# Optimization experiments

Hardware: AMD Instinct MI355X
Metric: run time of the kernel (lower is better)

The kernel has to match this reference:

```python
import jax, jax.numpy as jnp
import numpy as np

NEG = -10000000.0

def setup_inputs() -> dict:
    key0 = jax.random.key(0)
    ks = jax.random.split(key0, 5)
    B, XL, KL, D = 16, 1024, 512, 1024  # D = 2*rnn_dim
    return {
        "x": jax.random.normal(ks[0], (B, XL, D), dtype=jnp.float32),
        "x_mask": jnp.ones((B, XL), dtype=jnp.float32),
        "key": jax.random.normal(ks[1], (B, KL, D), dtype=jnp.float32),
        "key_mask": jnp.ones((B, KL), dtype=jnp.float32),
        "w_input": jax.random.normal(ks[2], (D,), dtype=jnp.float32) / np.sqrt(D),
        "w_key": jax.random.normal(ks[3], (D,), dtype=jnp.float32) / np.sqrt(D),
        "dot_w": jax.random.normal(ks[4], (D,), dtype=jnp.float32) / np.sqrt(D),
    }

def reference(x, x_mask, key, key_mask, w_input, w_key, dot_w):
    # Trilinear attention score S[b,i,j] = w_in.x_i + w_key.k_j + (x_i*dot_w).k_j
    x_logits = jnp.einsum('bxd,d->bx', x, w_input)      # [B, XL]
    key_logits = jnp.einsum('bkd,d->bk', key, w_key)    # [B, KL]
    S = (x_logits[:, :, None] + key_logits[:, None, :]
         + jnp.einsum('bxd,bkd->bxk', x * dot_w, key))  # [B, XL, KL]

    # x -> key attention with joint mask
    joint_mask = 1.0 - x_mask[:, :, None] * key_mask[:, None, :]
    masked_S = S + joint_mask * NEG
    attn = jax.nn.softmax(masked_S, axis=-1)
    x2key = jnp.einsum('bxk,bkd->bxd', attn, key)       # [B, XL, D]

    # key -> x attention: mask over key dim, max-reduce, masked softmax over x
    km = key_mask[:, None, :]
    S2 = S * km + (1.0 - km) * NEG                      # add_masked_value
    max_s = jnp.max(S2, axis=-1)                        # [B, XL]
    p = jax.nn.softmax(max_s * x_mask, axis=-1) * x_mask  # claf masked_softmax
    p = p / (jnp.sum(p, axis=-1, keepdims=True) + 1e-13)
    key2x = jnp.einsum('bx,bxd->bd', p, x)[:, None, :]  # [B, 1, D], broadcasts

    key2x_full = jnp.broadcast_to(key2x, x.shape)
    return jnp.concatenate([x, x2key, x * x2key, x * key2x_full], axis=-1)
```

## Files before the change

### kernel.cpp

```cpp
#include <hip/hip_runtime.h>
#include <hip/hip_fp16.h>

#define B_ 16
#define XL_ 1024
#define KL_ 512
#define D_ 1024
#define NEGC (-10000000.0f)

typedef _Float16 f16x8 __attribute__((ext_vector_type(8)));
typedef float f32x4 __attribute__((ext_vector_type(4)));
typedef unsigned short u16x8 __attribute__((ext_vector_type(8)));
typedef unsigned short u16x4 __attribute__((ext_vector_type(4)));

__device__ __forceinline__ unsigned short f2h(float f) {
  __half h = __float2half(f);
  return __half_as_ushort(h);
}

__global__ __launch_bounds__(256) void k_build(const float* __restrict__ key,
    const float* __restrict__ w_key, unsigned short* __restrict__ KQ2,
    unsigned short* __restrict__ KV2, float* __restrict__ klog) {
  __shared__ unsigned short tile[64][72];
  int bid = blockIdx.x;
  int b = bid >> 4;
  int ks = (bid >> 1) & 7;
  int dh = bid & 1;
  int tid = threadIdx.x;
  int kr = tid >> 2;
  int cq = tid & 3;
  const float* krow = key + ((size_t)(b * KL_ + ks * 64 + kr)) * D_;
  float klacc = 0.f;
  int dl = tid & 63, g = tid >> 6;

  for (int dt = dh * 8; dt < dh * 8 + 8; ++dt) {
#pragma unroll
    for (int j = 0; j < 4; ++j) {
      int c = dt * 64 + cq * 16 + j * 4;
      float4 v = *(const float4*)(krow + c);
      float4 w = *(const float4*)(w_key + c);
      klacc += v.x * w.x + v.y * w.y + v.z * w.z + v.w * w.w;
      u16x4 hv;
      hv[0] = f2h(v.x); hv[1] = f2h(v.y); hv[2] = f2h(v.z); hv[3] = f2h(v.w);
      *(u16x4*)(&tile[kr][cq * 16 + j * 4]) = hv;
    }
    __syncthreads();
#pragma unroll
    for (int dkc_l = 0; dkc_l < 2; ++dkc_l) {
      u16x8 hv = *(const u16x8*)(&tile[kr][dkc_l * 32 + cq * 8]);
      size_t dst = (((size_t)(b * 8 + ks) * 32 + (dt * 2 + dkc_l)) << 11)
                   + (size_t)(((kr >> 4) & 3) * 512 + (cq * 16 + (kr & 15)) * 8);
      *(u16x8*)(KQ2 + dst) = hv;
    }
    {
      int dglob = dt * 64 + dl;
      int wv_ = dglob >> 7, np = (dglob >> 4) & 7, l15v = dglob & 15;
#pragma unroll
      for (int kkc_l = 0; kkc_l < 2; ++kkc_l) {
        u16x8 hv;
#pragma unroll
        for (int h = 0; h < 8; ++h) hv[h] = tile[kkc_l * 32 + g * 8 + h][dl];
        size_t dst = (((size_t)(b * 8 + wv_) * 16 + (ks * 2 + kkc_l)) << 12)
                     + (size_t)(np * 512 + (g * 16 + l15v) * 8);
        *(u16x8*)(KV2 + dst) = hv;
      }
    }
    __syncthreads();
  }
  klacc += __shfl_xor(klacc, 1);
  klacc += __shfl_xor(klacc, 2);
  if (cq == 0) atomicAdd(&klog[b * KL_ + ks * 64 + kr], klacc);
}

__global__ __launch_bounds__(512, 4) void k_attn(
    const float* __restrict__ x, const float* __restrict__ x_mask,
    const float* __restrict__ key_mask, const float* __restrict__ dot_w,
    const float* __restrict__ w_input,
    const unsigned short* __restrict__ KQ2, const unsigned short* __restrict__ KV2,
    const float* __restrict__ klog,
    float* __restrict__ maxs, float* __restrict__ out) {
  __shared__ unsigned short Qall[32 * 1024];
  __shared__ float xlg[32];
  unsigned short* Pt = Qall;
  float* redA = (float*)(Qall + 16384);
  float* redB = redA + 256;
  float* redC = redB + 256;

  const int tid = threadIdx.x;
  const int wv = tid >> 6;
  const int lane = tid & 63;
  const int l15 = lane & 15, l4 = lane >> 4;
  const int r7 = l15 & 7;

  int bid = blockIdx.x;
  int b = (bid & 7) * 2 + (bid >> 8);
  int x0 = ((bid >> 3) & 31) * 32;

  const float* xB = x + ((size_t)b * XL_ + x0) * D_;

  {
    int row = tid >> 4;
    int cg = tid & 15;
    const float* sp = xB + (size_t)row * D_;
    float* outx = out + ((size_t)b * XL_ + x0 + row) * (size_t)(4 * D_);
    char* qrow = (char*)Qall + row * 2048;
    int rsw = row & 7;
    float xl = 0.f;
#pragma unroll
    for (int j = 0; j < 16; ++j) {
      int c4 = cg + j * 16;
      f32x4 v = *(const f32x4*)(sp + c4 * 4);
      f32x4 w = *(const f32x4*)(dot_w + c4 * 4);
      f32x4 wi = *(const f32x4*)(w_input + c4 * 4);
      xl += v[0] * wi[0] + v[1] * wi[1] + v[2] * wi[2] + v[3] * wi[3];
      __builtin_nontemporal_store(v, (f32x4*)(outx + c4 * 4));
      u16x4 hv;
      hv[0] = f2h(v[0] * w[0]); hv[1] = f2h(v[1] * w[1]);
      hv[2] = f2h(v[2] * w[2]); hv[3] = f2h(v[3] * w[3]);
      *(u16x4*)(qrow + (((c4 >> 1) ^ rsw) << 4) + ((c4 & 1) << 3)) = hv;
    }
    xl += __shfl_xor(xl, 1);
    xl += __shfl_xor(xl, 2);
    xl += __shfl_xor(xl, 4);
    xl += __shfl_xor(xl, 8);
    if (cg == 0) xlg[row] = xl;
  }
  __syncthreads();

  f32x4 acc[2][4];
#pragma unroll
  for (int m = 0; m < 2; ++m)
#pragma unroll
    for (int n = 0; n < 4; ++n) { f32x4 z = {0.f, 0.f, 0.f, 0.f}; acc[m][n] = z; }

  const unsigned short* KQ2w = KQ2 + (((size_t)(b * 8 + wv) * 32) << 11) + lane * 8;
  const char* qa0 = (char*)Qall + l15 * 2048;
  const char* qa1 = (char*)Qall + (16 + l15) * 2048;

#pragma unroll 4
  for (int dk = 0; dk < D_; dk += 32) {
    const unsigned short* cp = KQ2w + ((dk >> 5) << 11);
    f16x8 b0 = *(const f16x8*)(cp);
    f16x8 b1 = *(const f16x8*)(cp + 512);
    f16x8 b2 = *(const f16x8*)(cp + 1024);
    f16x8 b3 = *(const f16x8*)(cp + 1536);
    int c = (((dk >> 3) + l4) ^ r7) << 4;
    f16x8 a0 = *(const f16x8*)(qa0 + c);
    f16x8 a1 = *(const f16x8*)(qa1 + c);
    __builtin_amdgcn_s_setprio(1);
    acc[0][0] = __builtin_amdgcn_mfma_f32_16x16x32_f16(b0, a0, acc[0][0], 0, 0, 0);
    acc[1][0] = __builtin_amdgcn_mfma_f32_16x16x32_f16(b0, a1, acc[1][0], 0, 0, 0);
    acc[0][1] = __builtin_amdgcn_mfma_f32_16x16x32_f16(b1, a0, acc[0][1], 0, 0, 0);
    acc[1][1] = __builtin_amdgcn_mfma_f32_16x16x32_f16(b1, a1, acc[1][1], 0, 0, 0);
    acc[0][2] = __builtin_amdgcn_mfma_f32_16x16x32_f16(b2, a0, acc[0][2], 0, 0, 0);
    acc[1][2] = __builtin_amdgcn_mfma_f32_16x16x32_f16(b2, a1, acc[1][2], 0, 0, 0);
    acc[0][3] = __builtin_amdgcn_mfma_f32_16x16x32_f16(b3, a0, acc[0][3], 0, 0, 0);
    acc[1][3] = __builtin_amdgcn_mfma_f32_16x16x32_f16(b3, a1, acc[1][3], 0, 0, 0);
    __builtin_amdgcn_s_setprio(0);
  }
  __syncthreads();

  float xlv[2], xmv[2];
#pragma unroll
  for (int m = 0; m < 2; ++m) {
    int row = m * 16 + l15;
    xlv[m] = xlg[row];
    xmv[m] = x_mask[(size_t)b * XL_ + x0 + row];
  }
  f32x4 klv[4], kmv[4];
#pragma unroll
  for (int n = 0; n < 4; ++n) {
    int kb = wv * 64 + n * 16 + l4 * 4;
    klv[n] = *(const f32x4*)(klog + (size_t)b * KL_ + kb);
    kmv[n] = *(const f32x4*)(key_mask + (size_t)b * KL_ + kb);
  }
  float mxsm[2] = {-3.0e38f, -3.0e38f}, mxs2[2] = {-3.0e38f, -3.0e38f};
#pragma unroll
  for (int m = 0; m < 2; ++m)
#pragma unroll
    for (int n = 0; n < 4; ++n)
#pragma unroll
      for (int q = 0; q < 4; ++q) {
        float s = acc[m][n][q] + xlv[m] + klv[n][q];
        float sm = s + (1.f - xmv[m] * kmv[n][q]) * NEGC;
        float s2 = s * kmv[n][q] + (1.f - kmv[n][q]) * NEGC;
        mxsm[m] = fmaxf(mxsm[m], sm);
        mxs2[m] = fmaxf(mxs2[m], s2);
      }
#pragma unroll
  for (int m = 0; m < 2; ++m) {
    mxsm[m] = fmaxf(mxsm[m], __shfl_xor(mxsm[m], 16));
    mxsm[m] = fmaxf(mxsm[m], __shfl_xor(mxsm[m], 32));
    mxs2[m] = fmaxf(mxs2[m], __shfl_xor(mxs2[m], 16));
    mxs2[m] = fmaxf(mxs2[m], __shfl_xor(mxs2[m], 32));
  }
  if (l4 == 0) {
#pragma unroll
    for (int m = 0; m < 2; ++m) {
      redA[wv * 32 + m * 16 + l15] = mxsm[m];
      redB[wv * 32 + m * 16 + l15] = mxs2[m];
    }
  }
  __syncthreads();
  float gmx[2];
#pragma unroll
  for (int m = 0; m < 2; ++m) {
    int row = m * 16 + l15;
    float v = redA[row];
#pragma unroll
    for (int w = 1; w < 8; ++w) v = fmaxf(v, redA[w * 32 + row]);
    gmx[m] = v;
  }
  if (tid < 32) {
    float v = redB[tid];
#pragma unroll
    for (int w = 1; w < 8; ++w) v = fmaxf(v, redB[w * 32 + tid]);
    maxs[(size_t)b * XL_ + x0 + tid] = v;
  }
  float rs[2] = {0.f, 0.f};
#pragma unroll
  for (int m = 0; m < 2; ++m) {
    int row = m * 16 + l15;
    char* prow = (char*)Pt + row * 1024;
    int rsw = row & 7;
#pragma unroll
    for (int n = 0; n < 4; ++n) {
      int k = wv * 64 + n * 16 + l4 * 4;
      u16x4 pk;
#pragma unroll
      for (int q = 0; q < 4; ++q) {
        float s = acc[m][n][q] + xlv[m] + klv[n][q];
        float sm = s + (1.f - xmv[m] * kmv[n][q]) * NEGC;
        float e = __expf(sm - gmx[m]);
        rs[m] += e;
        pk[q] = f2h(e);
      }
      *(u16x4*)(prow + ((((k >> 3) ^ rsw) << 4) + ((k & 4) << 1))) = pk;
    }
  }
#pragma unroll
  for (int m = 0; m < 2; ++m) {
    rs[m] += __shfl_xor(rs[m], 16);
    rs[m] += __shfl_xor(rs[m], 32);
  }
  if (l4 == 0) {
#pragma unroll
    for (int m = 0; m < 2; ++m) redC[wv * 32 + m * 16 + l15] = rs[m];
  }
  __syncthreads();

  float dn[2];
#pragma unroll
  for (int m = 0; m < 2; ++m) {
    int row = m * 16 + l15;
    float sum = redC[row];
#pragma unroll
    for (int w = 1; w < 8; ++w) sum += redC[w * 32 + row];
    dn[m] = 1.f / sum;
  }
  size_t obase0 = ((size_t)b * XL_ + x0) * (size_t)(4 * D_);
  const char* pa0 = (char*)Pt + l15 * 1024;
  const char* pa1 = (char*)Pt + (16 + l15) * 1024;
  const unsigned short* KV2w = KV2 + (((size_t)(b * 8 + wv) * 16) << 12) + lane * 8;
#pragma unroll
  for (int sc = 0; sc < 2; ++sc) {
    int c0 = wv * 128 + sc * 64;
    f32x4 acc2[2][4];
#pragma unroll
    for (int m = 0; m < 2; ++m)
#pragma unroll
      for (int n = 0; n < 4; ++n) { f32x4 z = {0.f, 0.f, 0.f, 0.f}; acc2[m][n] = z; }
    const unsigned short* KV2s = KV2w + sc * 4 * 512;
#pragma unroll 4
    for (int kk = 0; kk < KL_; kk += 32) {
      const unsigned short* cp = KV2s + ((kk >> 5) << 12);
      f16x8 b0 = *(const f16x8*)(cp);
      f16x8 b1 = *(const f16x8*)(cp + 512);
      f16x8 b2 = *(const f16x8*)(cp + 1024);
      f16x8 b3 = *(const f16x8*)(cp + 1536);
      int c = ((((kk >> 3) + l4) ^ r7) << 4);
      f16x8 a0 = *(const f16x8*)(pa0 + c);
      f16x8 a1 = *(const f16x8*)(pa1 + c);
      __builtin_amdgcn_s_setprio(1);
      acc2[0][0] = __builtin_amdgcn_mfma_f32_16x16x32_f16(b0, a0, acc2[0][0], 0, 0, 0);
      acc2[1][0] = __builtin_amdgcn_mfma_f32_16x16x32_f16(b0, a1, acc2[1][0], 0, 0, 0);
      acc2[0][1] = __builtin_amdgcn_mfma_f32_16x16x32_f16(b1, a0, acc2[0][1], 0, 0, 0);
      acc2[1][1] = __builtin_amdgcn_mfma_f32_16x16x32_f16(b1, a1, acc2[1][1], 0, 0, 0);
      acc2[0][2] = __builtin_amdgcn_mfma_f32_16x16x32_f16(b2, a0, acc2[0][2], 0, 0, 0);
      acc2[1][2] = __builtin_amdgcn_mfma_f32_16x16x32_f16(b2, a1, acc2[1][2], 0, 0, 0);
      acc2[0][3] = __builtin_amdgcn_mfma_f32_16x16x32_f16(b3, a0, acc2[0][3], 0, 0, 0);
      acc2[1][3] = __builtin_amdgcn_mfma_f32_16x16x32_f16(b3, a1, acc2[1][3], 0, 0, 0);
      __builtin_amdgcn_s_setprio(0);
    }
#pragma unroll
    for (int m = 0; m < 2; ++m) {
      int row = m * 16 + l15;
      size_t ob = obase0 + (size_t)row * (4 * D_);
      const float* xr = xB + (size_t)row * D_;
#pragma unroll
      for (int n = 0; n < 4; ++n) {
        int col = c0 + n * 16 + l4 * 4;
        f32x4 v = acc2[m][n];
        v[0] *= dn[m]; v[1] *= dn[m]; v[2] *= dn[m]; v[3] *= dn[m];
        f32x4 xv = *(const f32x4*)(xr + col);
        __builtin_nontemporal_store(v, (f32x4*)(out + ob + D_ + col));
        f32x4 pv;
        pv[0] = v[0] * xv[0]; pv[1] = v[1] * xv[1];
        pv[2] = v[2] * xv[2]; pv[3] = v[3] * xv[3];
        __builtin_nontemporal_store(pv, (f32x4*)(out + ob + 2 * D_ + col));
      }
    }
  }
}

__global__ __launch_bounds__(256) void k_key2x_part(const float* __restrict__ x,
    const float* __restrict__ maxs, const float* __restrict__ x_mask,
    float* __restrict__ partial) {
  int b = blockIdx.x >> 4;
  int xc = blockIdx.x & 15;
  int tid = threadIdx.x;
  int wvi = tid >> 6, lane = tid & 63;
  __shared__ float r1[4], r2[4], r3[4];
  __shared__ float ps_all[XL_];
  const float* ms = maxs + (size_t)b * XL_;
  const float* xm = x_mask + (size_t)b * XL_;
  float tv[4], xmv[4];
  float vmax = -3.0e38f;
#pragma unroll
  for (int i = 0; i < 4; ++i) {
    int xi = i * 256 + tid;
    xmv[i] = xm[xi];
    tv[i] = ms[xi] * xmv[i];
    vmax = fmaxf(vmax, tv[i]);
  }
#pragma unroll
  for (int sh = 32; sh >= 1; sh >>= 1) vmax = fmaxf(vmax, __shfl_xor(vmax, sh));
  if (lane == 0) r1[wvi] = vmax;
  __syncthreads();
  float gmax = fmaxf(fmaxf(r1[0], r1[1]), fmaxf(r1[2], r1[3]));
  float e[4]; float es = 0.f;
#pragma unroll
  for (int i = 0; i < 4; ++i) { e[i] = __expf(tv[i] - gmax); es += e[i]; }
#pragma unroll
  for (int sh = 32; sh >= 1; sh >>= 1) es += __shfl_xor(es, sh);
  if (lane == 0) r2[wvi] = es;
  __syncthreads();
  float gsum = r2[0] + r2[1] + r2[2] + r2[3];
  float pv4[4]; float psum = 0.f;
#pragma unroll
  for (int i = 0; i < 4; ++i) { pv4[i] = e[i] / gsum * xmv[i]; psum += pv4[i]; }
#pragma unroll
  for (int sh = 32; sh >= 1; sh >>= 1) psum += __shfl_xor(psum, sh);
  if (lane == 0) r3[wvi] = psum;
  __syncthreads();
  float gps = r3[0] + r3[1] + r3[2] + r3[3];
  float inv = 1.f / (gps + 1e-13f);
#pragma unroll
  for (int i = 0; i < 4; ++i) ps_all[i * 256 + tid] = pv4[i] * inv;
  __syncthreads();
  const float* xb = x + ((size_t)b * XL_ + xc * 64) * D_;
  float acc0 = 0.f, acc1 = 0.f, acc2 = 0.f, acc3 = 0.f;
  int d = tid;
  const float* psl = ps_all + xc * 64;
  for (int xi = 0; xi < 64; ++xi) {
    float pv = psl[xi];
    const float* rp = xb + (size_t)xi * D_;
    acc0 += pv * __builtin_nontemporal_load(rp + d);
    acc1 += pv * __builtin_nontemporal_load(rp + d + 256);
    acc2 += pv * __builtin_nontemporal_load(rp + d + 512);
    acc3 += pv * __builtin_nontemporal_load(rp + d + 768);
  }
  float* pp = partial + (size_t)blockIdx.x * D_;
  pp[d] = acc0; pp[d + 256] = acc1; pp[d + 512] = acc2; pp[d + 768] = acc3;
}

__global__ __launch_bounds__(256) void k_key2x_red(const float* __restrict__ partial,
    float* __restrict__ k2x) {
  int idx = blockIdx.x * 256 + threadIdx.x;
  int b = idx >> 10;
  float s = 0.f;
#pragma unroll
  for (int xc = 0; xc < 16; ++xc)
    s += partial[((size_t)b * 16 + xc) * D_ + (idx & 1023)];
  k2x[idx] = s;
}

__global__ __launch_bounds__(256) void k_outfinal(const float* __restrict__ x,
    const float* __restrict__ k2x, float* __restrict__ out) {
  size_t t = (size_t)blockIdx.x * 256 + threadIdx.x;
  size_t base = t * 4;
  int b = (int)(base >> 20);
  int rem = (int)(base & ((1u << 20) - 1));
  int xr = rem >> 10;
  int d = rem & 1023;
  f32x4 xv = __builtin_nontemporal_load((const f32x4*)(x + base));
  f32x4 kv = *(const f32x4*)(k2x + (size_t)b * D_ + d);
  float* orow = out + ((size_t)b * XL_ + xr) * (size_t)(4 * D_);
  f32x4 pr;
  pr[0] = xv[0] * kv[0]; pr[1] = xv[1] * kv[1];
  pr[2] = xv[2] * kv[2]; pr[3] = xv[3] * kv[3];
  __builtin_nontemporal_store(pr, (f32x4*)(orow + 3 * D_ + d));
}

extern "C" void kernel_launch(void* const* d_in, const int* in_sizes, int n_in,
                              void* d_out, int out_size, void* d_ws, size_t ws_size,
                              hipStream_t stream) {
  (void)in_sizes; (void)n_in; (void)out_size; (void)ws_size;
  const float* x        = (const float*)d_in[0];
  const float* x_mask   = (const float*)d_in[1];
  const float* key      = (const float*)d_in[2];
  const float* key_mask = (const float*)d_in[3];
  const float* w_input  = (const float*)d_in[4];
  const float* w_key    = (const float*)d_in[5];
  const float* dot_w    = (const float*)d_in[6];
  float* out = (float*)d_out;
  char* ws = (char*)d_ws;

  unsigned short* KQ2 = (unsigned short*)ws;
  unsigned short* KV2 = (unsigned short*)(ws + (16u << 20));
  float* xlog = (float*)(ws + (32u << 20));
  float* klog = xlog + B_ * XL_;
  float* maxs = klog + B_ * KL_;
  float* pbuf = maxs + B_ * XL_;
  float* k2x  = pbuf + B_ * XL_;
  float* partial = (float*)ws;

  hipMemsetAsync(klog, 0, B_ * KL_ * sizeof(float), stream);
  k_build<<<dim3(B_ * 16), dim3(256), 0, stream>>>(key, w_key, KQ2, KV2, klog);
  k_attn<<<dim3(512), dim3(512), 0, stream>>>(x, x_mask, key_mask, dot_w, w_input,
                                              KQ2, KV2, klog, maxs, out);
  k_key2x_part<<<dim3(B_ * 16), dim3(256), 0, stream>>>(x, maxs, x_mask, partial);
  k_key2x_red<<<dim3(B_ * D_ / 256), dim3(256), 0, stream>>>(partial, k2x);
  k_outfinal<<<dim3(B_ * XL_ * D_ / 1024), dim3(256), 0, stream>>>(x, k2x, out);
}
```

Before: 172.8 us.

## Double attention block rows to 64 and move x copy into epilogue

Each k_attn block now handles 64 query rows instead of 32, so every K fragment loaded from global memory feeds four MFMA row tiles instead of two. This halves the grid to 256 blocks and doubles shared memory and accumulator registers, with launch bounds lowered to 2 blocks per CU. The copy of x into the first output slice moves from the prologue into the x2key epilogue, reusing the x values already loaded there. The nontemporal stores become ordinary stores. The larger tile risks register pressure and lower occupancy, and 256 blocks may leave some CUs idle.

Result: slower. 184.8 us (+6.9%).

```diff
diff --git a/kernel.cpp b/kernel.cpp
--- a/kernel.cpp
+++ b/kernel.cpp
@@ -71,19 +71,19 @@
   if (cq == 0) atomicAdd(&klog[b * KL_ + ks * 64 + kr], klacc);
 }
 
-__global__ __launch_bounds__(512, 4) void k_attn(
+__global__ __launch_bounds__(512, 2) void k_attn(
     const float* __restrict__ x, const float* __restrict__ x_mask,
     const float* __restrict__ key_mask, const float* __restrict__ dot_w,
     const float* __restrict__ w_input,
     const unsigned short* __restrict__ KQ2, const unsigned short* __restrict__ KV2,
     const float* __restrict__ klog,
     float* __restrict__ maxs, float* __restrict__ out) {
-  __shared__ unsigned short Qall[32 * 1024];
-  __shared__ float xlg[32];
+  __shared__ unsigned short Qall[64 * 1024];
+  __shared__ float xlg[64];
   unsigned short* Pt = Qall;
-  float* redA = (float*)(Qall + 16384);
-  float* redB = redA + 256;
-  float* redC = redB + 256;
+  float* redA = (float*)((char*)Qall + 65536);
+  float* redB = redA + 512;
+  float* redC = redB + 512;
 
   const int tid = threadIdx.x;
   const int wv = tid >> 6;
@@ -92,27 +92,25 @@
   const int r7 = l15 & 7;
 
   int bid = blockIdx.x;
-  int b = (bid & 7) * 2 + (bid >> 8);
-  int x0 = ((bid >> 3) & 31) * 32;
+  int b = (bid & 7) * 2 + (bid >> 7);
+  int x0 = ((bid >> 3) & 15) * 64;
 
   const float* xB = x + ((size_t)b * XL_ + x0) * D_;
 
   {
-    int row = tid >> 4;
-    int cg = tid & 15;
+    int row = tid >> 3;
+    int cg = tid & 7;
     const float* sp = xB + (size_t)row * D_;
-    float* outx = out + ((size_t)b * XL_ + x0 + row) * (size_t)(4 * D_);
     char* qrow = (char*)Qall + row * 2048;
     int rsw = row & 7;
     float xl = 0.f;
 #pragma unroll
-    for (int j = 0; j < 16; ++j) {
-      int c4 = cg + j * 16;
+    for (int j = 0; j < 32; ++j) {
+      int c4 = cg + j * 8;
       f32x4 v = *(const f32x4*)(sp + c4 * 4);
       f32x4 w = *(const f32x4*)(dot_w + c4 * 4);
       f32x4 wi = *(const f32x4*)(w_input + c4 * 4);
       xl += v[0] * wi[0] + v[1] * wi[1] + v[2] * wi[2] + v[3] * wi[3];
-      __builtin_nontemporal_store(v, (f32x4*)(outx + c4 * 4));
       u16x4 hv;
       hv[0] = f2h(v[0] * w[0]); hv[1] = f2h(v[1] * w[1]);
       hv[2] = f2h(v[2] * w[2]); hv[3] = f2h(v[3] * w[3]);
@@ -121,22 +119,23 @@
     xl += __shfl_xor(xl, 1);
     xl += __shfl_xor(xl, 2);
     xl += __shfl_xor(xl, 4);
-    xl += __shfl_xor(xl, 8);
     if (cg == 0) xlg[row] = xl;
   }
   __syncthreads();
 
-  f32x4 acc[2][4];
-#pragma unroll
-  for (int m = 0; m < 2; ++m)
+  f32x4 acc[4][4];
+#pragma unroll
+  for (int m = 0; m < 4; ++m)
 #pragma unroll
     for (int n = 0; n < 4; ++n) { f32x4 z = {0.f, 0.f, 0.f, 0.f}; acc[m][n] = z; }
 
   const unsigned short* KQ2w = KQ2 + (((size_t)(b * 8 + wv) * 32) << 11) + lane * 8;
   const char* qa0 = (char*)Qall + l15 * 2048;
   const char* qa1 = (char*)Qall + (16 + l15) * 2048;
-
-#pragma unroll 4
+  const char* qa2 = (char*)Qall + (32 + l15) * 2048;
+  const char* qa3 = (char*)Qall + (48 + l15) * 2048;
+
+#pragma unroll 2
   for (int dk = 0; dk < D_; dk += 32) {
     const unsigned short* cp = KQ2w + ((dk >> 5) << 11);
     f16x8 b0 = *(const f16x8*)(cp);
@@ -146,22 +145,32 @@
     int c = (((dk >> 3) + l4) ^ r7) << 4;
     f16x8 a0 = *(const f16x8*)(qa0 + c);
     f16x8 a1 = *(const f16x8*)(qa1 + c);
+    f16x8 a2 = *(const f16x8*)(qa2 + c);
+    f16x8 a3 = *(const f16x8*)(qa3 + c);
     __builtin_amdgcn_s_setprio(1);
     acc[0][0] = __builtin_amdgcn_mfma_f32_16x16x32_f16(b0, a0, acc[0][0], 0, 0, 0);
     acc[1][0] = __builtin_amdgcn_mfma_f32_16x16x32_f16(b0, a1, acc[1][0], 0, 0, 0);
+    acc[2][0] = __builtin_amdgcn_mfma_f32_16x16x32_f16(b0, a2, acc[2][0], 0, 0, 0);
+    acc[3][0] = __builtin_amdgcn_mfma_f32_16x16x32_f16(b0, a3, acc[3][0], 0, 0, 0);
     acc[0][1] = __builtin_amdgcn_mfma_f32_16x16x32_f16(b1, a0, acc[0][1], 0, 0, 0);
     acc[1][1] = __builtin_amdgcn_mfma_f32_16x16x32_f16(b1, a1, acc[1][1], 0, 0, 0);
+    acc[2][1] = __builtin_amdgcn_mfma_f32_16x16x32_f16(b1, a2, acc[2][1], 0, 0, 0);
+    acc[3][1] = __builtin_amdgcn_mfma_f32_16x16x32_f16(b1, a3, acc[3][1], 0, 0, 0);
     acc[0][2] = __builtin_amdgcn_mfma_f32_16x16x32_f16(b2, a0, acc[0][2], 0, 0, 0);
     acc[1][2] = __builtin_amdgcn_mfma_f32_16x16x32_f16(b2, a1, acc[1][2], 0, 0, 0);
+    acc[2][2] = __builtin_amdgcn_mfma_f32_16x16x32_f16(b2, a2, acc[2][2], 0, 0, 0);
+    acc[3][2] = __builtin_amdgcn_mfma_f32_16x16x32_f16(b2, a3, acc[3][2], 0, 0, 0);
     acc[0][3] = __builtin_amdgcn_mfma_f32_16x16x32_f16(b3, a0, acc[0][3], 0, 0, 0);
     acc[1][3] = __builtin_amdgcn_mfma_f32_16x16x32_f16(b3, a1, acc[1][3], 0, 0, 0);
+    acc[2][3] = __builtin_amdgcn_mfma_f32_16x16x32_f16(b3, a2, acc[2][3], 0, 0, 0);
+    acc[3][3] = __builtin_amdgcn_mfma_f32_16x16x32_f16(b3, a3, acc[3][3], 0, 0, 0);
     __builtin_amdgcn_s_setprio(0);
   }
   __syncthreads();
 
-  float xlv[2], xmv[2];
-#pragma unroll
-  for (int m = 0; m < 2; ++m) {
+  float xlv[4], xmv[4];
+#pragma unroll
+  for (int m = 0; m < 4; ++m) {
     int row = m * 16 + l15;
     xlv[m] = xlg[row];
     xmv[m] = x_mask[(size_t)b * XL_ + x0 + row];
@@ -173,9 +182,11 @@
     klv[n] = *(const f32x4*)(klog + (size_t)b * KL_ + kb);
     kmv[n] = *(const f32x4*)(key_mask + (size_t)b * KL_ + kb);
   }
-  float mxsm[2] = {-3.0e38f, -3.0e38f}, mxs2[2] = {-3.0e38f, -3.0e38f};
-#pragma unroll
-  for (int m = 0; m < 2; ++m)
+  float mxsm[4], mxs2[4];
+#pragma unroll
+  for (int m = 0; m < 4; ++m) { mxsm[m] = -3.0e38f; mxs2[m] = -3.0e38f; }
+#pragma unroll
+  for (int m = 0; m < 4; ++m)
 #pragma unroll
     for (int n = 0; n < 4; ++n)
 #pragma unroll
@@ -187,7 +198,7 @@
         mxs2[m] = fmaxf(mxs2[m], s2);
       }
 #pragma unroll
-  for (int m = 0; m < 2; ++m) {
+  for (int m = 0; m < 4; ++m) {
     mxsm[m] = fmaxf(mxsm[m], __shfl_xor(mxsm[m], 16));
     mxsm[m] = fmaxf(mxsm[m], __shfl_xor(mxsm[m], 32));
     mxs2[m] = fmaxf(mxs2[m], __shfl_xor(mxs2[m], 16));
@@ -195,30 +206,30 @@
   }
   if (l4 == 0) {
 #pragma unroll
-    for (int m = 0; m < 2; ++m) {
-      redA[wv * 32 + m * 16 + l15] = mxsm[m];
-      redB[wv * 32 + m * 16 + l15] = mxs2[m];
-    }
-  }
-  __syncthreads();
-  float gmx[2];
-#pragma unroll
-  for (int m = 0; m < 2; ++m) {
+    for (int m = 0; m < 4; ++m) {
+      redA[wv * 64 + m * 16 + l15] = mxsm[m];
+      redB[wv * 64 + m * 16 + l15] = mxs2[m];
+    }
+  }
+  __syncthreads();
+  float gmx[4];
+#pragma unroll
+  for (int m = 0; m < 4; ++m) {
     int row = m * 16 + l15;
     float v = redA[row];
 #pragma unroll
-    for (int w = 1; w < 8; ++w) v = fmaxf(v, redA[w * 32 + row]);
+    for (int w = 1; w < 8; ++w) v = fmaxf(v, redA[w * 64 + row]);
     gmx[m] = v;
   }
-  if (tid < 32) {
+  if (tid < 64) {
     float v = redB[tid];
 #pragma unroll
-    for (int w = 1; w < 8; ++w) v = fmaxf(v, redB[w * 32 + tid]);
+    for (int w = 1; w < 8; ++w) v = fmaxf(v, redB[w * 64 + tid]);
     maxs[(size_t)b * XL_ + x0 + tid] = v;
   }
-  float rs[2] = {0.f, 0.f};
-#pragma unroll
-  for (int m = 0; m < 2; ++m) {
+  float rs[4] = {0.f, 0.f, 0.f, 0.f};
+#pragma unroll
+  for (int m = 0; m < 4; ++m) {
     int row = m * 16 + l15;
     char* prow = (char*)Pt + row * 1024;
     int rsw = row & 7;
@@ -238,39 +249,41 @@
     }
   }
 #pragma unroll
-  for (int m = 0; m < 2; ++m) {
+  for (int m = 0; m < 4; ++m) {
     rs[m] += __shfl_xor(rs[m], 16);
     rs[m] += __shfl_xor(rs[m], 32);
   }
   if (l4 == 0) {
 #pragma unroll
-    for (int m = 0; m < 2; ++m) redC[wv * 32 + m * 16 + l15] = rs[m];
-  }
-  __syncthreads();
-
-  float dn[2];
-#pragma unroll
-  for (int m = 0; m < 2; ++m) {
+    for (int m = 0; m < 4; ++m) redC[wv * 64 + m * 16 + l15] = rs[m];
+  }
+  __syncthreads();
+
+  float dn[4];
+#pragma unroll
+  for (int m = 0; m < 4; ++m) {
     int row = m * 16 + l15;
     float sum = redC[row];
 #pragma unroll
-    for (int w = 1; w < 8; ++w) sum += redC[w * 32 + row];
+    for (int w = 1; w < 8; ++w) sum += redC[w * 64 + row];
     dn[m] = 1.f / sum;
   }
   size_t obase0 = ((size_t)b * XL_ + x0) * (size_t)(4 * D_);
   const char* pa0 = (char*)Pt + l15 * 1024;
   const char* pa1 = (char*)Pt + (16 + l15) * 1024;
+  const char* pa2 = (char*)Pt + (32 + l15) * 1024;
+  const char* pa3 = (char*)Pt + (48 + l15) * 1024;
   const unsigned short* KV2w = KV2 + (((size_t)(b * 8 + wv) * 16) << 12) + lane * 8;
 #pragma unroll
   for (int sc = 0; sc < 2; ++sc) {
     int c0 = wv * 128 + sc * 64;
-    f32x4 acc2[2][4];
-#pragma unroll
-    for (int m = 0; m < 2; ++m)
+    f32x4 acc2[4][4];
+#pragma unroll
+    for (int m = 0; m < 4; ++m)
 #pragma unroll
       for (int n = 0; n < 4; ++n) { f32x4 z = {0.f, 0.f, 0.f, 0.f}; acc2[m][n] = z; }
     const unsigned short* KV2s = KV2w + sc * 4 * 512;
-#pragma unroll 4
+#pragma unroll 2
     for (int kk = 0; kk < KL_; kk += 32) {
       const unsigned short* cp = KV2s + ((kk >> 5) << 12);
       f16x8 b0 = *(const f16x8*)(cp);
@@ -280,19 +293,29 @@
       int c = ((((kk >> 3) + l4) ^ r7) << 4);
       f16x8 a0 = *(const f16x8*)(pa0 + c);
       f16x8 a1 = *(const f16x8*)(pa1 + c);
+      f16x8 a2 = *(const f16x8*)(pa2 + c);
+      f16x8 a3 = *(const f16x8*)(pa3 + c);
       __builtin_amdgcn_s_setprio(1);
       acc2[0][0] = __builtin_amdgcn_mfma_f32_16x16x32_f16(b0, a0, acc2[0][0], 0, 0, 0);
       acc2[1][0] = __builtin_amdgcn_mfma_f32_16x16x32_f16(b0, a1, acc2[1][0], 0, 0, 0);
+      acc2[2][0] = __builtin_amdgcn_mfma_f32_16x16x32_f16(b0, a2, acc2[2][0], 0, 0, 0);
+      acc2[3][0] = __builtin_amdgcn_mfma_f32_16x16x32_f16(b0, a3, acc2[3][0], 0, 0, 0);
       acc2[0][1] = __builtin_amdgcn_mfma_f32_16x16x32_f16(b1, a0, acc2[0][1], 0, 0, 0);
       acc2[1][1] = __builtin_amdgcn_mfma_f32_16x16x32_f16(b1, a1, acc2[1][1], 0, 0, 0);
+      acc2[2][1] = __builtin_amdgcn_mfma_f32_16x16x32_f16(b1, a2, acc2[2][1], 0, 0, 0);
+      acc2[3][1] = __builtin_amdgcn_mfma_f32_16x16x32_f16(b1, a3, acc2[3][1], 0, 0, 0);
       acc2[0][2] = __builtin_amdgcn_mfma_f32_16x16x32_f16(b2, a0, acc2[0][2], 0, 0, 0);
       acc2[1][2] = __builtin_amdgcn_mfma_f32_16x16x32_f16(b2, a1, acc2[1][2], 0, 0, 0);
+      acc2[2][2] = __builtin_amdgcn_mfma_f32_16x16x32_f16(b2, a2, acc2[2][2], 0, 0, 0);
+      acc2[3][2] = __builtin_amdgcn_mfma_f32_16x16x32_f16(b2, a3, acc2[3][2], 0, 0, 0);
       acc2[0][3] = __builtin_amdgcn_mfma_f32_16x16x32_f16(b3, a0, acc2[0][3], 0, 0, 0);
       acc2[1][3] = __builtin_amdgcn_mfma_f32_16x16x32_f16(b3, a1, acc2[1][3], 0, 0, 0);
+      acc2[2][3] = __builtin_amdgcn_mfma_f32_16x16x32_f16(b3, a2, acc2[2][3], 0, 0, 0);
+      acc2[3][3] = __builtin_amdgcn_mfma_f32_16x16x32_f16(b3, a3, acc2[3][3], 0, 0, 0);
       __builtin_amdgcn_s_setprio(0);
     }
 #pragma unroll
-    for (int m = 0; m < 2; ++m) {
+    for (int m = 0; m < 4; ++m) {
       int row = m * 16 + l15;
       size_t ob = obase0 + (size_t)row * (4 * D_);
       const float* xr = xB + (size_t)row * D_;
@@ -302,11 +325,12 @@
         f32x4 v = acc2[m][n];
         v[0] *= dn[m]; v[1] *= dn[m]; v[2] *= dn[m]; v[3] *= dn[m];
         f32x4 xv = *(const f32x4*)(xr + col);
-        __builtin_nontemporal_store(v, (f32x4*)(out + ob + D_ + col));
+        *(f32x4*)(out + ob + col) = xv;
+        *(f32x4*)(out + ob + D_ + col) = v;
         f32x4 pv;
         pv[0] = v[0] * xv[0]; pv[1] = v[1] * xv[1];
         pv[2] = v[2] * xv[2]; pv[3] = v[3] * xv[3];
-        __builtin_nontemporal_store(pv, (f32x4*)(out + ob + 2 * D_ + col));
+        *(f32x4*)(out + ob + 2 * D_ + col) = pv;
       }
     }
   }
@@ -426,7 +450,7 @@
 
   hipMemsetAsync(klog, 0, B_ * KL_ * sizeof(float), stream);
   k_build<<<dim3(B_ * 16), dim3(256), 0, stream>>>(key, w_key, KQ2, KV2, klog);
-  k_attn<<<dim3(512), dim3(512), 0, stream>>>(x, x_mask, key_mask, dot_w, w_input,
+  k_attn<<<dim3(256), dim3(512), 0, stream>>>(x, x_mask, key_mask, dot_w, w_input,
                                               KQ2, KV2, klog, maxs, out);
   k_key2x_part<<<dim3(B_ * 16), dim3(256), 0, stream>>>(x, maxs, x_mask, partial);
   k_key2x_red<<<dim3(B_ * D_ / 256), dim3(256), 0, stream>>>(partial, k2x);
```

## Move x copy and x*x2key output writes from attention into final streaming kernel

Applied to the files above, without the earlier changes.

The attention kernel no longer writes the x passthrough slice or the x*x2key product, and no longer re-reads x in its epilogue. The final elementwise kernel now produces three output slices: it stores x, reads x2key back from the output buffer to form x*x2key, and writes x*key2x. The aim is to take store traffic out of the MFMA-heavy attention kernel and run it as a pure streaming pass. The cost is an extra global read of the x2key slice. The key loads in k_build also become nontemporal.

Result: faster. 169.1 us (-2.1%).

```diff
diff --git a/kernel.cpp b/kernel.cpp
--- a/kernel.cpp
+++ b/kernel.cpp
@@ -36,11 +36,11 @@
 #pragma unroll
     for (int j = 0; j < 4; ++j) {
       int c = dt * 64 + cq * 16 + j * 4;
-      float4 v = *(const float4*)(krow + c);
-      float4 w = *(const float4*)(w_key + c);
-      klacc += v.x * w.x + v.y * w.y + v.z * w.z + v.w * w.w;
+      f32x4 v = __builtin_nontemporal_load((const f32x4*)(krow + c));
+      f32x4 w = *(const f32x4*)(w_key + c);
+      klacc += v[0] * w[0] + v[1] * w[1] + v[2] * w[2] + v[3] * w[3];
       u16x4 hv;
-      hv[0] = f2h(v.x); hv[1] = f2h(v.y); hv[2] = f2h(v.z); hv[3] = f2h(v.w);
+      hv[0] = f2h(v[0]); hv[1] = f2h(v[1]); hv[2] = f2h(v[2]); hv[3] = f2h(v[3]);
       *(u16x4*)(&tile[kr][cq * 16 + j * 4]) = hv;
     }
     __syncthreads();
@@ -101,7 +101,6 @@
     int row = tid >> 4;
     int cg = tid & 15;
     const float* sp = xB + (size_t)row * D_;
-    float* outx = out + ((size_t)b * XL_ + x0 + row) * (size_t)(4 * D_);
     char* qrow = (char*)Qall + row * 2048;
     int rsw = row & 7;
     float xl = 0.f;
@@ -112,7 +111,6 @@
       f32x4 w = *(const f32x4*)(dot_w + c4 * 4);
       f32x4 wi = *(const f32x4*)(w_input + c4 * 4);
       xl += v[0] * wi[0] + v[1] * wi[1] + v[2] * wi[2] + v[3] * wi[3];
-      __builtin_nontemporal_store(v, (f32x4*)(outx + c4 * 4));
       u16x4 hv;
       hv[0] = f2h(v[0] * w[0]); hv[1] = f2h(v[1] * w[1]);
       hv[2] = f2h(v[2] * w[2]); hv[3] = f2h(v[3] * w[3]);
@@ -295,18 +293,12 @@
     for (int m = 0; m < 2; ++m) {
       int row = m * 16 + l15;
       size_t ob = obase0 + (size_t)row * (4 * D_);
-      const float* xr = xB + (size_t)row * D_;
 #pragma unroll
       for (int n = 0; n < 4; ++n) {
         int col = c0 + n * 16 + l4 * 4;
         f32x4 v = acc2[m][n];
         v[0] *= dn[m]; v[1] *= dn[m]; v[2] *= dn[m]; v[3] *= dn[m];
-        f32x4 xv = *(const f32x4*)(xr + col);
         __builtin_nontemporal_store(v, (f32x4*)(out + ob + D_ + col));
-        f32x4 pv;
-        pv[0] = v[0] * xv[0]; pv[1] = v[1] * xv[1];
-        pv[2] = v[2] * xv[2]; pv[3] = v[3] * xv[3];
-        __builtin_nontemporal_store(pv, (f32x4*)(out + ob + 2 * D_ + col));
       }
     }
   }
@@ -384,7 +376,7 @@
   k2x[idx] = s;
 }
 
-__global__ __launch_bounds__(256) void k_outfinal(const float* __restrict__ x,
+__global__ __launch_bounds__(256) void k_mega(const float* __restrict__ x,
     const float* __restrict__ k2x, float* __restrict__ out) {
   size_t t = (size_t)blockIdx.x * 256 + threadIdx.x;
   size_t base = t * 4;
@@ -395,10 +387,16 @@
   f32x4 xv = __builtin_nontemporal_load((const f32x4*)(x + base));
   f32x4 kv = *(const f32x4*)(k2x + (size_t)b * D_ + d);
   float* orow = out + ((size_t)b * XL_ + xr) * (size_t)(4 * D_);
-  f32x4 pr;
-  pr[0] = xv[0] * kv[0]; pr[1] = xv[1] * kv[1];
-  pr[2] = xv[2] * kv[2]; pr[3] = xv[3] * kv[3];
-  __builtin_nontemporal_store(pr, (f32x4*)(orow + 3 * D_ + d));
+  f32x4 x2 = __builtin_nontemporal_load((const f32x4*)(orow + D_ + d));
+  __builtin_nontemporal_store(xv, (f32x4*)(orow + d));
+  f32x4 p2;
+  p2[0] = xv[0] * x2[0]; p2[1] = xv[1] * x2[1];
+  p2[2] = xv[2] * x2[2]; p2[3] = xv[3] * x2[3];
+  __builtin_nontemporal_store(p2, (f32x4*)(orow + 2 * D_ + d));
+  f32x4 p3;
+  p3[0] = xv[0] * kv[0]; p3[1] = xv[1] * kv[1];
+  p3[2] = xv[2] * kv[2]; p3[3] = xv[3] * kv[3];
+  __builtin_nontemporal_store(p3, (f32x4*)(orow + 3 * D_ + d));
 }
 
 extern "C" void kernel_launch(void* const* d_in, const int* in_sizes, int n_in,
@@ -430,5 +428,5 @@
                                               KQ2, KV2, klog, maxs, out);
   k_key2x_part<<<dim3(B_ * 16), dim3(256), 0, stream>>>(x, maxs, x_mask, partial);
   k_key2x_red<<<dim3(B_ * D_ / 256), dim3(256), 0, stream>>>(partial, k2x);
-  k_outfinal<<<dim3(B_ * XL_ * D_ / 1024), dim3(256), 0, stream>>>(x, k2x, out);
-}
+  k_mega<<<dim3(B_ * XL_ * D_ / 1024), dim3(256), 0, stream>>>(x, k2x, out);
+}
```
